# Kernel optimization log

Hardware: AMD Instinct MI355X
Metric: run time of the kernel (lower is better)

## Reference

```python
import jax, jax.numpy as jnp
import numpy as np

N_NODES = 100000
N_EDGES = 1600000
IN_DIM = 256
OUT_DIM = 64
LEAKY_SLOPE = 0.01  # torch F.leaky_relu default


def setup_inputs() -> dict:
    key = jax.random.key(0)
    k1, k2, k3, k4, k5 = jax.random.split(key, 5)
    h = jax.random.normal(k1, (N_NODES, IN_DIM), dtype=jnp.float32)
    W_fc = jax.random.normal(k2, (IN_DIM, OUT_DIM), dtype=jnp.float32) * (1.0 / np.sqrt(IN_DIM))
    a_attn = jax.random.normal(k3, (2 * OUT_DIM,), dtype=jnp.float32) * (1.0 / np.sqrt(2 * OUT_DIM))
    edge_src = jax.random.randint(k4, (N_EDGES,), 0, N_NODES, dtype=jnp.int32)
    edge_dst = jax.random.randint(k5, (N_EDGES,), 0, N_NODES, dtype=jnp.int32)
    return {"h": h, "W_fc": W_fc, "a_attn": a_attn, "edge_src": edge_src, "edge_dst": edge_dst}


def reference(h, W_fc, a_attn, edge_src, edge_dst):
    # z = fc(h)  (no bias)
    z = h @ W_fc                                   # [N, D]
    # edge attention: leaky_relu(concat(z_src, z_dst) @ a)
    # split a into src/dst halves -> node-level projections (same math, no concat)
    el = z @ a_attn[:OUT_DIM]                      # [N]
    er = z @ a_attn[OUT_DIM:]                      # [N]
    e = jax.nn.leaky_relu(el[edge_src] + er[edge_dst], negative_slope=LEAKY_SLOPE)  # [E]
    # segment softmax over destination-node mailboxes
    m = jax.ops.segment_max(e, edge_dst, num_segments=N_NODES)   # [N]
    ex = jnp.exp(e - m[edge_dst])                                # [E]
    s = jax.ops.segment_sum(ex, edge_dst, num_segments=N_NODES)  # [N]
    alpha = ex / s[edge_dst]                                     # [E]
    # weighted scatter-sum of neighbor features
    h_out = jax.ops.segment_sum(alpha[:, None] * z[edge_src], edge_dst, num_segments=N_NODES)  # [N, D]
    # heads != 1 branch: ELU (dropout = 0 in eval)
    return jax.nn.elu(h_out)
```

## Files before the change

### kernel.cpp

```cpp
#include <hip/hip_runtime.h>
#include <hip/hip_bf16.h>

#define IN_DIM 256
#define OUT_DIM 64
#define CHUNK 8192
#define BSH 8
#define P2CAP 6144

typedef short bf16x8 __attribute__((ext_vector_type(8)));
typedef float f32x4 __attribute__((ext_vector_type(4)));

__device__ inline unsigned short f2bf(float x) {
  unsigned int u = __float_as_uint(x);
  return (unsigned short)((u + 0x7FFFu + ((u >> 16) & 1u)) >> 16);
}

__global__ __launch_bounds__(256) void k_prep(const float* __restrict__ W,
                                              unsigned short* __restrict__ Wbf,
                                              int* __restrict__ tot) {
  int f = blockIdx.x * 256 + threadIdx.x;
  if (f < 512) tot[f] = 0;
  int kc = f >> 8, ct = (f >> 6) & 3, q = (f >> 4) & 3, nq = f & 15;
  int col = ct * 16 + nq, k0 = kc * 32 + q * 8;
  unsigned short v[8];
#pragma unroll
  for (int j = 0; j < 8; ++j) v[j] = f2bf(W[(size_t)(k0 + j) * OUT_DIM + col]);
  *(uint4*)(Wbf + (size_t)f * 8) = *(uint4*)v;
}

__global__ __launch_bounds__(256) void k_gemm(const float* __restrict__ h,
                                              const unsigned short* __restrict__ Wbf,
                                              const float* __restrict__ a,
                                              unsigned short* __restrict__ zb,
                                              float* __restrict__ el,
                                              float* __restrict__ er, int n,
                                              const int* __restrict__ dst,
                                              int* __restrict__ tot, int E,
                                              int nbuck) {
  __shared__ unsigned short Ab[64][264];
  __shared__ int hist[512];
  const int t = threadIdx.x;
  const int base = blockIdx.x * 64;

#pragma unroll
  for (int i = 0; i < 16; ++i) {
    int f = i * 256 + t;
    int r = f >> 6, c4 = f & 63;
    int row = base + r;
    float4 v = make_float4(0.f, 0.f, 0.f, 0.f);
    if (row < n) v = *(const float4*)(h + (size_t)row * IN_DIM + c4 * 4);
    unsigned int p0 = (unsigned int)f2bf(v.x) | ((unsigned int)f2bf(v.y) << 16);
    unsigned int p1 = (unsigned int)f2bf(v.z) | ((unsigned int)f2bf(v.w) << 16);
    *(uint2*)&Ab[r][c4 * 4] = make_uint2(p0, p1);
  }
  __syncthreads();

  const int w = t >> 6, lane = t & 63, nq = lane & 15, q = lane >> 4;

  f32x4 acc[4];
#pragma unroll
  for (int ct = 0; ct < 4; ++ct) acc[ct] = (f32x4){0.f, 0.f, 0.f, 0.f};

#pragma unroll
  for (int kc = 0; kc < 8; ++kc) {
    bf16x8 af = *(const bf16x8*)&Ab[w * 16 + nq][kc * 32 + q * 8];
#pragma unroll
    for (int ct = 0; ct < 4; ++ct) {
      bf16x8 bfr = *(const bf16x8*)(Wbf + (size_t)((kc * 4 + ct) * 64 + lane) * 8);
      acc[ct] = __builtin_amdgcn_mfma_f32_16x16x32_bf16(af, bfr, acc[ct], 0, 0, 0);
    }
  }

  float a1[4], a2[4];
#pragma unroll
  for (int ct = 0; ct < 4; ++ct) {
    a1[ct] = a[ct * 16 + nq];
    a2[ct] = a[OUT_DIM + ct * 16 + nq];
  }
#pragma unroll
  for (int r = 0; r < 4; ++r) {
    int orow = base + w * 16 + q * 4 + r;
    float p1 = 0.f, p2 = 0.f;
#pragma unroll
    for (int ct = 0; ct < 4; ++ct) {
      float v = acc[ct][r];
      p1 += v * a1[ct];
      p2 += v * a2[ct];
      if (orow < n) zb[(size_t)orow * OUT_DIM + ct * 16 + nq] = f2bf(v);
    }
    p1 += __shfl_xor(p1, 1); p1 += __shfl_xor(p1, 2);
    p1 += __shfl_xor(p1, 4); p1 += __shfl_xor(p1, 8);
    p2 += __shfl_xor(p2, 1); p2 += __shfl_xor(p2, 2);
    p2 += __shfl_xor(p2, 4); p2 += __shfl_xor(p2, 8);
    if (orow < n && nq == 0) { el[orow] = p1; er[orow] = p2; }
  }

  hist[t] = 0;
  hist[t + 256] = 0;
  __syncthreads();
  int e0 = blockIdx.x * 1024 + t * 4;
  if (e0 + 4 <= E) {
    int4 d4 = *(const int4*)(dst + e0);
    atomicAdd(&hist[d4.x >> BSH], 1);
    atomicAdd(&hist[d4.y >> BSH], 1);
    atomicAdd(&hist[d4.z >> BSH], 1);
    atomicAdd(&hist[d4.w >> BSH], 1);
  } else {
#pragma unroll
    for (int k = 0; k < 4; ++k) {
      int e = e0 + k;
      if (e < E) atomicAdd(&hist[dst[e] >> BSH], 1);
    }
  }
  __syncthreads();
  for (int i = t; i < nbuck; i += 256)
    if (hist[i]) atomicAdd(&tot[i], hist[i]);
}

__global__ __launch_bounds__(256) void k_scanT(const int* __restrict__ tot,
                                               int* __restrict__ pbeg,
                                               int* __restrict__ gcur, int nbuck) {
  __shared__ int wtot[4];
  int t = threadIdx.x;
  int d0 = (2 * t < nbuck) ? tot[2 * t] : 0;
  int d1 = (2 * t + 1 < nbuck) ? tot[2 * t + 1] : 0;
  int tsum = d0 + d1;
  int lane = t & 63, w = t >> 6;
  int incl = tsum;
  for (int o = 1; o < 64; o <<= 1) {
    int u = __shfl_up(incl, o);
    if (lane >= o) incl += u;
  }
  if (lane == 63) wtot[w] = incl;
  __syncthreads();
  int woff = 0;
  for (int i = 0; i < 4; ++i)
    if (i < w) woff += wtot[i];
  int ex = woff + incl - tsum;
  pbeg[2 * t] = ex;
  gcur[2 * t] = ex;
  pbeg[2 * t + 1] = ex + d0;
  gcur[2 * t + 1] = ex + d0;
}

__global__ __launch_bounds__(512) void k_part(const int* __restrict__ src,
                                              const int* __restrict__ dst,
                                              int* __restrict__ gcur,
                                              int* __restrict__ pairs, int E,
                                              int nbuck) {
  __shared__ int hist[512];
  __shared__ int excl[512];
  __shared__ int cur[512];
  __shared__ int rbase[512];
  __shared__ int stage[CHUNK];
  __shared__ unsigned short sbk[CHUNK];
  __shared__ int wtot[8];
  const int t = threadIdx.x, b = blockIdx.x;
  const int beg = b * CHUNK;
  const int cnt = min(CHUNK, E - beg);

  hist[t] = 0;
  __syncthreads();

  int dv[16], sv[16];
#pragma unroll
  for (int k = 0; k < 16; ++k) {
    int i = k * 512 + t;
    dv[k] = -1;
    if (i < cnt) {
      dv[k] = dst[beg + i];
      sv[k] = src[beg + i];
      atomicAdd(&hist[dv[k] >> BSH], 1);
    }
  }
  __syncthreads();

  {
    int v = hist[t];
    int lane = t & 63, w = t >> 6;
    int incl = v;
    for (int o = 1; o < 64; o <<= 1) {
      int u = __shfl_up(incl, o);
      if (lane >= o) incl += u;
    }
    if (lane == 63) wtot[w] = incl;
    __syncthreads();
    int woff = 0;
    for (int i = 0; i < 8; ++i)
      if (i < w) woff += wtot[i];
    int ex = woff + incl - v;
    excl[t] = ex;
    cur[t] = ex;
    if (t < nbuck && v > 0) rbase[t] = atomicAdd(&gcur[t], v);
  }
  __syncthreads();

#pragma unroll
  for (int k = 0; k < 16; ++k) {
    if (dv[k] >= 0) {
      int bk = dv[k] >> BSH;
      int r = atomicAdd(&cur[bk], 1);
      stage[r] = ((dv[k] & ((1 << BSH) - 1)) << 24) | sv[k];
      sbk[r] = (unsigned short)bk;
    }
  }
  __syncthreads();

  for (int i = t; i < cnt; i += 512) {
    int bk = sbk[i];
    pairs[rbase[bk] + (i - excl[bk])] = stage[i];
  }
}

__global__ __launch_bounds__(1024) void k_p2agg(const int* __restrict__ pairs,
                                                const int* __restrict__ tot,
                                                const int* __restrict__ pbeg,
                                                const float* __restrict__ el,
                                                const float* __restrict__ er,
                                                const unsigned short* __restrict__ zb,
                                                float* __restrict__ out, int n) {
  __shared__ int deg[256];
  __shared__ int loff[257];
  __shared__ int cur[256];
  __shared__ int stage[P2CAP];
  __shared__ int wtot[4];
  const int t = threadIdx.x, b = blockIdx.x;
  const int beg = pbeg[b];
  const int cnt = tot[b];

  if (t < 256) deg[t] = 0;
  __syncthreads();

  int pv[6];
#pragma unroll
  for (int k = 0; k < 6; ++k) {
    int i = k * 1024 + t;
    pv[k] = 0;
    if (i < cnt) {
      pv[k] = pairs[beg + i];
      atomicAdd(&deg[((unsigned)pv[k]) >> 24], 1);
    }
  }
  __syncthreads();

  int v = 0, inc = 0;
  const int lane = t & 63, w = t >> 6;
  if (t < 256) {
    v = deg[t];
    inc = v;
    for (int o = 1; o < 64; o <<= 1) {
      int u = __shfl_up(inc, o);
      if (lane >= o) inc += u;
    }
    if (lane == 63) wtot[w] = inc;
  }
  __syncthreads();
  if (t < 256) {
    int woff = 0;
    for (int i = 0; i < 4; ++i)
      if (i < w) woff += wtot[i];
    int ex = woff + inc - v;
    loff[t] = ex;
    cur[t] = ex;
    if (t == 255) loff[256] = ex + v;
  }
  __syncthreads();

#pragma unroll
  for (int k = 0; k < 6; ++k) {
    int i = k * 1024 + t;
    if (i < cnt) {
      int r = atomicAdd(&cur[((unsigned)pv[k]) >> 24], 1);
      if (r < P2CAP) stage[r] = pv[k] & 0xFFFFFF;
    }
  }
  __syncthreads();

  const int g = t >> 4;
  const int cq = (t & 15) * 4;
#pragma unroll
  for (int round = 0; round < 4; ++round) {
    int nl = round * 64 + g;
    int node = (b << BSH) + nl;
    if (node >= n) continue;
    int jb = loff[nl], je = loff[nl + 1];
    float erd = er[node];
    float ax = 0.f, ay = 0.f, az = 0.f, aw = 0.f, ssum = 0.f;
    int j = jb;
    for (; j + 4 <= je; j += 4) {
      int s0 = stage[j], s1 = stage[j + 1], s2 = stage[j + 2], s3 = stage[j + 3];
      uint2 z0 = *(const uint2*)(zb + (s0 << 6) + cq);
      uint2 z1 = *(const uint2*)(zb + (s1 << 6) + cq);
      uint2 z2 = *(const uint2*)(zb + (s2 << 6) + cq);
      uint2 z3 = *(const uint2*)(zb + (s3 << 6) + cq);
      float x0 = el[s0] + erd, x1 = el[s1] + erd;
      float x2 = el[s2] + erd, x3 = el[s3] + erd;
      x0 = x0 > 0.f ? x0 : 0.01f * x0;
      x1 = x1 > 0.f ? x1 : 0.01f * x1;
      x2 = x2 > 0.f ? x2 : 0.01f * x2;
      x3 = x3 > 0.f ? x3 : 0.01f * x3;
      float e0 = __expf(x0), e1 = __expf(x1), e2 = __expf(x2), e3 = __expf(x3);
      ssum += (e0 + e1) + (e2 + e3);
      ax += e0 * __uint_as_float(z0.x << 16) + e1 * __uint_as_float(z1.x << 16) +
            e2 * __uint_as_float(z2.x << 16) + e3 * __uint_as_float(z3.x << 16);
      ay += e0 * __uint_as_float(z0.x & 0xFFFF0000u) + e1 * __uint_as_float(z1.x & 0xFFFF0000u) +
            e2 * __uint_as_float(z2.x & 0xFFFF0000u) + e3 * __uint_as_float(z3.x & 0xFFFF0000u);
      az += e0 * __uint_as_float(z0.y << 16) + e1 * __uint_as_float(z1.y << 16) +
            e2 * __uint_as_float(z2.y << 16) + e3 * __uint_as_float(z3.y << 16);
      aw += e0 * __uint_as_float(z0.y & 0xFFFF0000u) + e1 * __uint_as_float(z1.y & 0xFFFF0000u) +
            e2 * __uint_as_float(z2.y & 0xFFFF0000u) + e3 * __uint_as_float(z3.y & 0xFFFF0000u);
    }
    for (; j < je; ++j) {
      int s = stage[j];
      uint2 zv = *(const uint2*)(zb + (s << 6) + cq);
      float x = el[s] + erd;
      x = x > 0.f ? x : 0.01f * x;
      float ex = __expf(x);
      ssum += ex;
      ax += ex * __uint_as_float(zv.x << 16);
      ay += ex * __uint_as_float(zv.x & 0xFFFF0000u);
      az += ex * __uint_as_float(zv.y << 16);
      aw += ex * __uint_as_float(zv.y & 0xFFFF0000u);
    }
    float4 o = make_float4(0.f, 0.f, 0.f, 0.f);
    if (je > jb) {
      float inv = 1.f / ssum;
      ax *= inv; ay *= inv; az *= inv; aw *= inv;
      o.x = ax > 0.f ? ax : __expf(ax) - 1.f;
      o.y = ay > 0.f ? ay : __expf(ay) - 1.f;
      o.z = az > 0.f ? az : __expf(az) - 1.f;
      o.w = aw > 0.f ? aw : __expf(aw) - 1.f;
    }
    *(float4*)(out + ((size_t)node << 6) + cq) = o;
  }
}

extern "C" void kernel_launch(void* const* d_in, const int* in_sizes, int n_in,
                              void* d_out, int out_size, void* d_ws, size_t ws_size,
                              hipStream_t stream) {
  const float* h = (const float*)d_in[0];
  const float* W = (const float*)d_in[1];
  const float* a = (const float*)d_in[2];
  const int* src = (const int*)d_in[3];
  const int* dst = (const int*)d_in[4];
  const int n = in_sizes[0] / IN_DIM;
  const int E = in_sizes[3];
  float* out = (float*)d_out;

  const int b1 = (E + CHUNK - 1) / CHUNK;
  const int nbuck = (n + (1 << BSH) - 1) >> BSH;

  char* ws = (char*)d_ws;
  auto alloc = [&](size_t bytes) {
    char* p = ws;
    ws += (bytes + 15) & ~(size_t)15;
    return p;
  };
  unsigned short* Wbf = (unsigned short*)alloc(16384 * 2);
  unsigned short* zb = (unsigned short*)alloc((size_t)n * OUT_DIM * 2);
  float* el = (float*)alloc((size_t)n * 4);
  float* er = (float*)alloc((size_t)n * 4);
  int* tot = (int*)alloc(512 * 4);
  int* pbeg = (int*)alloc(512 * 4);
  int* gcur = (int*)alloc(512 * 4);
  int* pairs = (int*)alloc((size_t)E * 4);

  k_prep<<<8, 256, 0, stream>>>(W, Wbf, tot);
  k_gemm<<<(n + 63) / 64, 256, 0, stream>>>(h, Wbf, a, zb, el, er, n, dst, tot, E, nbuck);
  k_scanT<<<1, 256, 0, stream>>>(tot, pbeg, gcur, nbuck);
  k_part<<<b1, 512, 0, stream>>>(src, dst, gcur, pairs, E, nbuck);
  k_p2agg<<<nbuck, 1024, 0, stream>>>(pairs, tot, pbeg, el, er, zb, out, n);
}
```

Before: 257.1 us.

## Load h tile directly to LDS as fp32 with swizzle, preload W fragments

The GEMM kernel now streams the fp32 h tile straight from global memory into LDS with global_load_lds. It uses an XOR swizzle on 16-byte chunks to avoid bank conflicts, and converts to bf16 only when reading MFMA fragments. All W fragments are hoisted into registers before the loop. This removes the register round-trip and per-element conversion on the load path. In exchange it doubles LDS use to 64 KB per block, which may lower occupancy, and adds register pressure from holding 32 bf16x8 fragments.

Measured after the change: 242.4 us. 5.7% less time.

```diff
diff --git a/kernel.cpp b/kernel.cpp
--- a/kernel.cpp
+++ b/kernel.cpp
@@ -14,6 +14,11 @@
   unsigned int u = __float_as_uint(x);
   return (unsigned short)((u + 0x7FFFu + ((u >> 16) & 1u)) >> 16);
 }
+
+#define GLOAD_LDS16(gp, lp)                                                        \
+  __builtin_amdgcn_global_load_lds(                                                \
+      (const __attribute__((address_space(1))) unsigned int*)(gp),                 \
+      (__attribute__((address_space(3))) unsigned int*)(lp), 16, 0, 0)
 
 __global__ __launch_bounds__(256) void k_prep(const float* __restrict__ W,
                                               unsigned short* __restrict__ Wbf,
@@ -37,38 +42,54 @@
                                               const int* __restrict__ dst,
                                               int* __restrict__ tot, int E,
                                               int nbuck) {
-  __shared__ unsigned short Ab[64][264];
+  __shared__ __align__(16) float Af[64 * 256];
   __shared__ int hist[512];
   const int t = threadIdx.x;
   const int base = blockIdx.x * 64;
+  const int w = t >> 6, lane = t & 63, nq = lane & 15, q = lane >> 4;
+
+  bf16x8 wf[8][4];
+#pragma unroll
+  for (int kc = 0; kc < 8; ++kc)
+#pragma unroll
+    for (int ct = 0; ct < 4; ++ct)
+      wf[kc][ct] = *(const bf16x8*)(Wbf + (((kc * 4 + ct) * 64 + lane) << 3));
 
 #pragma unroll
   for (int i = 0; i < 16; ++i) {
     int f = i * 256 + t;
-    int r = f >> 6, c4 = f & 63;
-    int row = base + r;
-    float4 v = make_float4(0.f, 0.f, 0.f, 0.f);
-    if (row < n) v = *(const float4*)(h + (size_t)row * IN_DIM + c4 * 4);
-    unsigned int p0 = (unsigned int)f2bf(v.x) | ((unsigned int)f2bf(v.y) << 16);
-    unsigned int p1 = (unsigned int)f2bf(v.z) | ((unsigned int)f2bf(v.w) << 16);
-    *(uint2*)&Ab[r][c4 * 4] = make_uint2(p0, p1);
-  }
-  __syncthreads();
-
-  const int w = t >> 6, lane = t & 63, nq = lane & 15, q = lane >> 4;
+    int row = f >> 6;
+    int cb = (f & 63) * 16;
+    int gcb = cb ^ ((row & 7) << 4);
+    int grow = base + row;
+    const char* gp = (grow < n) ? (const char*)h + ((size_t)grow * 1024 + gcb)
+                                : (const char*)h;
+    char* lp = (char*)Af + (size_t)(i * 4096 + w * 1024);
+    GLOAD_LDS16(gp, lp);
+  }
+  __syncthreads();
 
   f32x4 acc[4];
 #pragma unroll
   for (int ct = 0; ct < 4; ++ct) acc[ct] = (f32x4){0.f, 0.f, 0.f, 0.f};
 
+  const int rowb = w * 16 + nq;
+  const char* Arow = (const char*)Af + rowb * 1024;
+  const int sw = (rowb & 7) << 4;
+
 #pragma unroll
   for (int kc = 0; kc < 8; ++kc) {
-    bf16x8 af = *(const bf16x8*)&Ab[w * 16 + nq][kc * 32 + q * 8];
-#pragma unroll
-    for (int ct = 0; ct < 4; ++ct) {
-      bf16x8 bfr = *(const bf16x8*)(Wbf + (size_t)((kc * 4 + ct) * 64 + lane) * 8);
-      acc[ct] = __builtin_amdgcn_mfma_f32_16x16x32_bf16(af, bfr, acc[ct], 0, 0, 0);
-    }
+    int c0 = kc * 128 + q * 32;
+    float4 lo = *(const float4*)(Arow + (c0 ^ sw));
+    float4 hi = *(const float4*)(Arow + ((c0 + 16) ^ sw));
+    bf16x8 af;
+    af[0] = (short)f2bf(lo.x); af[1] = (short)f2bf(lo.y);
+    af[2] = (short)f2bf(lo.z); af[3] = (short)f2bf(lo.w);
+    af[4] = (short)f2bf(hi.x); af[5] = (short)f2bf(hi.y);
+    af[6] = (short)f2bf(hi.z); af[7] = (short)f2bf(hi.w);
+#pragma unroll
+    for (int ct = 0; ct < 4; ++ct)
+      acc[ct] = __builtin_amdgcn_mfma_f32_16x16x32_bf16(af, wf[kc][ct], acc[ct], 0, 0, 0);
   }
 
   float a1[4], a2[4];
```

## Load A fragments directly to registers and stage W in LDS via global_load_lds

Applied to the files above, without the earlier changes.

The GEMM kernel no longer stages the h tile through shared memory. Each lane now loads its own A fragment straight from global memory into registers and converts it to bf16 in place. The bf16 weight matrix is instead copied into LDS with the async global_load_lds builtin and read from there for the MFMA B operand. Histogram zeroing moves ahead of the single barrier, and launch bounds request 4 blocks per CU. This removes one LDS round trip and a barrier for A and replaces repeated global W reads with LDS reads, at the cost of per-lane strided global loads of h and higher register pressure.

Result: faster. 249.9 us (-2.8%).

```diff
diff --git a/kernel.cpp b/kernel.cpp
--- a/kernel.cpp
+++ b/kernel.cpp
@@ -14,6 +14,11 @@
   unsigned int u = __float_as_uint(x);
   return (unsigned short)((u + 0x7FFFu + ((u >> 16) & 1u)) >> 16);
 }
+
+#define GLOAD_LDS16(gp, lp)                                                        \
+  __builtin_amdgcn_global_load_lds(                                                \
+      (const __attribute__((address_space(1))) unsigned int*)(gp),                 \
+      (__attribute__((address_space(3))) unsigned int*)(lp), 16, 0, 0)
 
 __global__ __launch_bounds__(256) void k_prep(const float* __restrict__ W,
                                               unsigned short* __restrict__ Wbf,
@@ -28,46 +33,56 @@
   *(uint4*)(Wbf + (size_t)f * 8) = *(uint4*)v;
 }
 
-__global__ __launch_bounds__(256) void k_gemm(const float* __restrict__ h,
-                                              const unsigned short* __restrict__ Wbf,
-                                              const float* __restrict__ a,
-                                              unsigned short* __restrict__ zb,
-                                              float* __restrict__ el,
-                                              float* __restrict__ er, int n,
-                                              const int* __restrict__ dst,
-                                              int* __restrict__ tot, int E,
-                                              int nbuck) {
-  __shared__ unsigned short Ab[64][264];
+__global__ __launch_bounds__(256, 4) void k_gemm(const float* __restrict__ h,
+                                                 const unsigned short* __restrict__ Wbf,
+                                                 const float* __restrict__ a,
+                                                 unsigned short* __restrict__ zb,
+                                                 float* __restrict__ el,
+                                                 float* __restrict__ er, int n,
+                                                 const int* __restrict__ dst,
+                                                 int* __restrict__ tot, int E,
+                                                 int nbuck) {
+  __shared__ __align__(16) unsigned short Wlds[16384];
   __shared__ int hist[512];
   const int t = threadIdx.x;
-  const int base = blockIdx.x * 64;
-
-#pragma unroll
-  for (int i = 0; i < 16; ++i) {
-    int f = i * 256 + t;
-    int r = f >> 6, c4 = f & 63;
-    int row = base + r;
-    float4 v = make_float4(0.f, 0.f, 0.f, 0.f);
-    if (row < n) v = *(const float4*)(h + (size_t)row * IN_DIM + c4 * 4);
-    unsigned int p0 = (unsigned int)f2bf(v.x) | ((unsigned int)f2bf(v.y) << 16);
-    unsigned int p1 = (unsigned int)f2bf(v.z) | ((unsigned int)f2bf(v.w) << 16);
-    *(uint2*)&Ab[r][c4 * 4] = make_uint2(p0, p1);
-  }
-  __syncthreads();
-
   const int w = t >> 6, lane = t & 63, nq = lane & 15, q = lane >> 4;
 
+#pragma unroll
+  for (int i = 0; i < 8; ++i) {
+    const char* gp = (const char*)Wbf + (size_t)(i * 256 + t) * 16;
+    char* lp = (char*)Wlds + (i * 4096 + w * 1024);
+    GLOAD_LDS16(gp, lp);
+  }
+  hist[t] = 0;
+  hist[t + 256] = 0;
+  __syncthreads();
+
+  const int tile = blockIdx.x * 4 + w;
+  const int arow = tile * 16 + nq;
+  const float* Ap = h + (size_t)min(arow, n - 1) * IN_DIM + q * 8;
+
+  float4 alo[8], ahi[8];
+#pragma unroll
+  for (int kc = 0; kc < 8; ++kc) {
+    alo[kc] = *(const float4*)(Ap + kc * 32);
+    ahi[kc] = *(const float4*)(Ap + kc * 32 + 4);
+  }
+
   f32x4 acc[4];
 #pragma unroll
   for (int ct = 0; ct < 4; ++ct) acc[ct] = (f32x4){0.f, 0.f, 0.f, 0.f};
 
 #pragma unroll
   for (int kc = 0; kc < 8; ++kc) {
-    bf16x8 af = *(const bf16x8*)&Ab[w * 16 + nq][kc * 32 + q * 8];
+    bf16x8 af;
+    af[0] = (short)f2bf(alo[kc].x); af[1] = (short)f2bf(alo[kc].y);
+    af[2] = (short)f2bf(alo[kc].z); af[3] = (short)f2bf(alo[kc].w);
+    af[4] = (short)f2bf(ahi[kc].x); af[5] = (short)f2bf(ahi[kc].y);
+    af[6] = (short)f2bf(ahi[kc].z); af[7] = (short)f2bf(ahi[kc].w);
 #pragma unroll
     for (int ct = 0; ct < 4; ++ct) {
-      bf16x8 bfr = *(const bf16x8*)(Wbf + (size_t)((kc * 4 + ct) * 64 + lane) * 8);
-      acc[ct] = __builtin_amdgcn_mfma_f32_16x16x32_bf16(af, bfr, acc[ct], 0, 0, 0);
+      bf16x8 wfr = *(const bf16x8*)&Wlds[(size_t)((kc * 4 + ct) * 64 + lane) * 8];
+      acc[ct] = __builtin_amdgcn_mfma_f32_16x16x32_bf16(af, wfr, acc[ct], 0, 0, 0);
     }
   }
 
@@ -79,7 +94,7 @@
   }
 #pragma unroll
   for (int r = 0; r < 4; ++r) {
-    int orow = base + w * 16 + q * 4 + r;
+    int orow = tile * 16 + q * 4 + r;
     float p1 = 0.f, p2 = 0.f;
 #pragma unroll
     for (int ct = 0; ct < 4; ++ct) {
@@ -95,9 +110,6 @@
     if (orow < n && nq == 0) { el[orow] = p1; er[orow] = p2; }
   }
 
-  hist[t] = 0;
-  hist[t + 256] = 0;
-  __syncthreads();
   int e0 = blockIdx.x * 1024 + t * 4;
   if (e0 + 4 <= E) {
     int4 d4 = *(const int4*)(dst + e0);
```
